# Optimization experiments

Hardware: AMD Instinct MI355X
Metric: run time of the kernel (lower is better)

Reference implementation:

```python
import jax, jax.numpy as jnp
import numpy as np

B, T, D, N = 64, 256, 32, 64  # batch, seq_len, input_dim, n_units
INIT_STD = 0.02


def setup_inputs() -> dict:
    key = jax.random.key(0)
    ks = jax.random.split(key, 13)
    x = jax.random.normal(ks[0], (B, T, D), dtype=jnp.float32)
    p = lambda k, shape: jax.random.normal(k, shape, dtype=jnp.float32) * INIT_STD
    return {
        "x": x,
        "W_j": p(ks[1], (D, N, N)), "W_i": p(ks[2], (D, N, N)),
        "W_f": p(ks[3], (D, N, N)), "W_o": p(ks[4], (D, N, N)),
        "U_j": p(ks[5], (D, 1, N)), "U_i": p(ks[6], (D, 1, N)),
        "U_f": p(ks[7], (D, 1, N)), "U_o": p(ks[8], (D, 1, N)),
        "b_j": p(ks[9], (D, N)), "b_i": p(ks[10], (D, N)),
        "b_f": p(ks[11], (D, N)), "b_o": p(ks[12], (D, N)),
    }


def reference(x, W_j, W_i, W_f, W_o, U_j, U_i, U_f, U_o, b_j, b_i, b_f, b_o):
    # x: [B, T, D]; per-input-variable LSTM with state [B, D, N].
    b = x.shape[0]
    d, _, n = W_j.shape
    # 'bij,jik->bjk' with i==1 is an outer product: x_t[b,d] * U[d,0,:]
    Uj, Ui, Uf, Uo = U_j[:, 0, :], U_i[:, 0, :], U_f[:, 0, :], U_o[:, 0, :]

    def step(carry, x_t):  # x_t: [B, D]
        h, c = carry  # each [B, D, N]
        xe = x_t[:, :, None]  # [B, D, 1]
        gate = lambda W, U, bb: jnp.einsum('bdn,dnm->bdm', h, W) + xe * U + bb
        j = jnp.tanh(gate(W_j, Uj, b_j))
        i = jax.nn.sigmoid(gate(W_i, Ui, b_i))
        f = jax.nn.sigmoid(gate(W_f, Uf, b_f))
        o = jax.nn.sigmoid(gate(W_o, Uo, b_o))
        c = c * f + i * j
        h = o * jnp.tanh(c)
        return (h, c), h

    h0 = jnp.zeros((b, d, n), dtype=x.dtype)
    (h_T, c_T), outs = jax.lax.scan(step, (h0, h0), jnp.swapaxes(x, 0, 1))
    outputs = jnp.swapaxes(outs, 0, 1)  # [B, T, D, N]
    return (outputs, (h_T, c_T))
```

## Files before the change

kernel.cpp:

```cpp
#include <hip/hip_runtime.h>
#include <hip/hip_bf16.h>
#include <stdint.h>


typedef __attribute__((ext_vector_type(8))) __bf16 bf16x8;
typedef __attribute__((ext_vector_type(4))) float f32x4;

union FragU { uint4 u; bf16x8 v; };

__device__ __forceinline__ float fast_sigmoid(float x) {
    float e = __builtin_amdgcn_exp2f(-1.4426950408889634f * x);
    return __builtin_amdgcn_rcpf(1.0f + e);
}
__device__ __forceinline__ float fast_tanh(float x) {
    float e = __builtin_amdgcn_exp2f(2.8853900817779268f * x);
    return 1.0f - 2.0f * __builtin_amdgcn_rcpf(1.0f + e);
}

__global__ __launch_bounds__(256, 2) void lstm_kernel(
    const float* __restrict__ x,
    const float* __restrict__ Wj, const float* __restrict__ Wi,
    const float* __restrict__ Wf, const float* __restrict__ Wo,
    const float* __restrict__ Uj, const float* __restrict__ Ui,
    const float* __restrict__ Uf, const float* __restrict__ Uo,
    const float* __restrict__ bj, const float* __restrict__ bi,
    const float* __restrict__ bf, const float* __restrict__ bo,
    float* __restrict__ out)
{
    constexpr int T = 256, D = 32, N = 64, B = 64;
    const int bid   = blockIdx.x;
    const int d     = bid >> 4;
    const int btile = bid & 15;
    const int tid   = threadIdx.x;
    const int w     = tid >> 6;
    const int lane  = tid & 63;
    const int g     = lane >> 4;
    const int li    = lane & 15;
    const int mcol  = w * 16 + li;

    __shared__ __align__(16) __bf16 hbuf[2][4][64];
    __shared__ float xs[4][256];

    for (int idx = tid; idx < 2 * 4 * 64; idx += 256)
        (&hbuf[0][0][0])[idx] = (__bf16)0.0f;
    for (int idx = tid; idx < 4 * 256; idx += 256) {
        int bl = idx >> 8, t = idx & 255;
        xs[bl][t] = x[((size_t)(btile * 4 + bl) * T + t) * D + d];
    }

    const float* Wg[4] = { Wj, Wi, Wf, Wo };
    const float* Ug[4] = { Uj, Ui, Uf, Uo };
    const float* Bg[4] = { bj, bi, bf, bo };
    FragU wfrag[4][2];
    float uv[4], bv[4];
    #pragma unroll
    for (int G = 0; G < 4; ++G) {
        uv[G] = Ug[G][d * N + mcol];
        bv[G] = Bg[G][d * N + mcol];
        const float* base = Wg[G] + (size_t)d * N * N + mcol;
        #pragma unroll
        for (int f = 0; f < 2; ++f) {
            const int k0 = f * 32 + g * 8;
            bf16x8 tmp;
            #pragma unroll
            for (int j = 0; j < 8; ++j)
                tmp[j] = (__bf16)base[(size_t)(k0 + j) * N];
            wfrag[G][f].v = tmp;
        }
    }

    f32x4 acc[4];
    #pragma unroll
    for (int G = 0; G < 4; ++G)
        acc[G] = f32x4{ bv[G], bv[G], bv[G], bv[G] };

    const int cm = mcol >> 3;
    const int woff = (((cm + 2 * g) & 7) << 3) | (mcol & 7);
    __bf16* hw0 = &hbuf[0][g][0] + woff;
    __bf16* hw1 = &hbuf[1][g][0] + woff;

    const int rr = li >> 2;
    const int p0 = (g + 2 * rr) & 7;
    const int p1 = (g + 4 + 2 * rr) & 7;
    const uint4* ra00 = (const uint4*)&hbuf[0][rr][p0 << 3];
    const uint4* ra01 = (const uint4*)&hbuf[1][rr][p0 << 3];
    const uint4* ra10 = (const uint4*)&hbuf[0][rr][p1 << 3];
    const uint4* ra11 = (const uint4*)&hbuf[1][rr][p1 << 3];

    __syncthreads();

    if (((bid >> 3) ^ (bid >> 8)) & 1)
        asm volatile("s_sleep 6" ::: "memory");

    float c0 = 0.f, h0 = 0.f;
    const int gb = btile * 4 + g;
    uint32_t oidx = (uint32_t)gb * (T * D * N) + (uint32_t)(d * N + mcol);

    #pragma unroll 1
    for (int t = 0; t < T; t += 8) {
        const float4 xa = *(const float4*)&xs[g][t];
        const float4 xb = *(const float4*)&xs[g][t + 4];
        #pragma unroll
        for (int uu = 0; uu < 8; ++uu) {
            __builtin_amdgcn_s_setprio(1);
            const int rb = uu & 1;
            FragU a0, a1;
            a0.u = *(rb ? ra01 : ra00);
            a1.u = *(rb ? ra11 : ra10);
            const float xv = (uu < 4) ? xa[uu] : xb[uu - 4];
            #pragma unroll
            for (int G = 0; G < 4; ++G)
                acc[G][0] = __builtin_fmaf(xv, uv[G], bv[G]);
            #pragma unroll
            for (int G = 0; G < 4; ++G) {
                acc[G] = __builtin_amdgcn_mfma_f32_16x16x32_bf16(a0.v, wfrag[G][0].v, acc[G], 0, 0, 0);
                acc[G] = __builtin_amdgcn_mfma_f32_16x16x32_bf16(a1.v, wfrag[G][1].v, acc[G], 0, 0, 0);
            }
            const float jj = fast_tanh   (acc[0][0]);
            const float ii = fast_sigmoid(acc[1][0]);
            const float ff = fast_sigmoid(acc[2][0]);
            const float oo = fast_sigmoid(acc[3][0]);
            c0 = __builtin_fmaf(c0, ff, ii * jj);
            h0 = oo * fast_tanh(c0);
            __builtin_amdgcn_s_setprio(0);
            *(rb ? hw0 : hw1) = (__bf16)h0;
            out[oidx] = h0;
            oidx += D * N;
            asm volatile("s_waitcnt lgkmcnt(0)" ::: "memory");
            __builtin_amdgcn_s_barrier();
        }
    }

    const size_t baseH = (size_t)B * T * D * N;
    const size_t baseC = baseH + (size_t)B * D * N;
    const size_t i0 = ((size_t)gb * D + d) * N + mcol;
    out[baseH + i0] = h0;
    out[baseC + i0] = c0;
}

extern "C" void kernel_launch(void* const* d_in, const int* in_sizes, int n_in,
                              void* d_out, int out_size, void* d_ws, size_t ws_size,
                              hipStream_t stream) {
    lstm_kernel<<<dim3(512), dim3(256), 0, stream>>>(
        (const float*)d_in[0],
        (const float*)d_in[1], (const float*)d_in[2],
        (const float*)d_in[3], (const float*)d_in[4],
        (const float*)d_in[5], (const float*)d_in[6],
        (const float*)d_in[7], (const float*)d_in[8],
        (const float*)d_in[9], (const float*)d_in[10],
        (const float*)d_in[11], (const float*)d_in[12],
        (float*)d_out);
}
```

Before: 80.46 us.

## Process eight batch rows per block using two MFMA accumulator rows

Each block now handles 8 batch rows instead of 4, so each thread carries two independent LSTM states in accumulator rows 0 and 1 of the same MFMA. The grid is halved to 256 blocks (one per CU on MI355X), the h buffer is padded to 72 columns in place of the XOR swizzle, and the setprio and staggered-sleep tricks are removed. This halves the number of serial recurrences per CU and doubles the useful rows per MFMA. In exchange each step does twice the gate math and global stores per thread, and occupancy is lower.

```diff
diff --git a/kernel.cpp b/kernel.cpp
--- a/kernel.cpp
+++ b/kernel.cpp
@@ -17,7 +17,7 @@
     return 1.0f - 2.0f * __builtin_amdgcn_rcpf(1.0f + e);
 }
 
-__global__ __launch_bounds__(256, 2) void lstm_kernel(
+__global__ __launch_bounds__(256, 1) void lstm_kernel(
     const float* __restrict__ x,
     const float* __restrict__ Wj, const float* __restrict__ Wi,
     const float* __restrict__ Wf, const float* __restrict__ Wo,
@@ -29,23 +29,23 @@
 {
     constexpr int T = 256, D = 32, N = 64, B = 64;
     const int bid   = blockIdx.x;
-    const int d     = bid >> 4;
-    const int btile = bid & 15;
+    const int d     = bid >> 3;
+    const int btile = bid & 7;
     const int tid   = threadIdx.x;
     const int w     = tid >> 6;
     const int lane  = tid & 63;
-    const int g     = lane >> 4;
+    const int q     = lane >> 4;
     const int li    = lane & 15;
     const int mcol  = w * 16 + li;
 
-    __shared__ __align__(16) __bf16 hbuf[2][4][64];
-    __shared__ float xs[4][256];
+    __shared__ __align__(16) __bf16 hbuf[2][8][72];
+    __shared__ __align__(16) float xs[8][256];
 
-    for (int idx = tid; idx < 2 * 4 * 64; idx += 256)
+    for (int idx = tid; idx < 2 * 8 * 72; idx += 256)
         (&hbuf[0][0][0])[idx] = (__bf16)0.0f;
-    for (int idx = tid; idx < 4 * 256; idx += 256) {
+    for (int idx = tid; idx < 8 * 256; idx += 256) {
         int bl = idx >> 8, t = idx & 255;
-        xs[bl][t] = x[((size_t)(btile * 4 + bl) * T + t) * D + d];
+        xs[bl][t] = x[((size_t)(btile * 8 + bl) * T + t) * D + d];
     }
 
     const float* Wg[4] = { Wj, Wi, Wf, Wo };
@@ -60,7 +60,7 @@
         const float* base = Wg[G] + (size_t)d * N * N + mcol;
         #pragma unroll
         for (int f = 0; f < 2; ++f) {
-            const int k0 = f * 32 + g * 8;
+            const int k0 = f * 32 + q * 8;
             bf16x8 tmp;
             #pragma unroll
             for (int j = 0; j < 8; ++j)
@@ -74,58 +74,68 @@
     for (int G = 0; G < 4; ++G)
         acc[G] = f32x4{ bv[G], bv[G], bv[G], bv[G] };
 
-    const int cm = mcol >> 3;
-    const int woff = (((cm + 2 * g) & 7) << 3) | (mcol & 7);
-    __bf16* hw0 = &hbuf[0][g][0] + woff;
-    __bf16* hw1 = &hbuf[1][g][0] + woff;
+    const int bb0 = 2 * q, bb1 = 2 * q + 1;
+    __bf16* hw0a = &hbuf[0][bb0][mcol];
+    __bf16* hw0b = &hbuf[0][bb1][mcol];
+    __bf16* hw1a = &hbuf[1][bb0][mcol];
+    __bf16* hw1b = &hbuf[1][bb1][mcol];
 
-    const int rr = li >> 2;
-    const int p0 = (g + 2 * rr) & 7;
-    const int p1 = (g + 4 + 2 * rr) & 7;
-    const uint4* ra00 = (const uint4*)&hbuf[0][rr][p0 << 3];
-    const uint4* ra01 = (const uint4*)&hbuf[1][rr][p0 << 3];
-    const uint4* ra10 = (const uint4*)&hbuf[0][rr][p1 << 3];
-    const uint4* ra11 = (const uint4*)&hbuf[1][rr][p1 << 3];
+    const int rr = 2 * (li >> 2) + (li & 1);
+    const uint4* ra00 = (const uint4*)&hbuf[0][rr][q * 8];
+    const uint4* ra01 = (const uint4*)&hbuf[1][rr][q * 8];
+    const uint4* ra10 = (const uint4*)&hbuf[0][rr][32 + q * 8];
+    const uint4* ra11 = (const uint4*)&hbuf[1][rr][32 + q * 8];
 
     __syncthreads();
 
-    if (((bid >> 3) ^ (bid >> 8)) & 1)
-        asm volatile("s_sleep 6" ::: "memory");
-
-    float c0 = 0.f, h0 = 0.f;
-    const int gb = btile * 4 + g;
-    uint32_t oidx = (uint32_t)gb * (T * D * N) + (uint32_t)(d * N + mcol);
+    float c0a = 0.f, h0a = 0.f, c0b = 0.f, h0b = 0.f;
+    const int gb0 = btile * 8 + bb0;
+    const int gb1 = gb0 + 1;
+    uint32_t oidx0 = (uint32_t)gb0 * (T * D * N) + (uint32_t)(d * N + mcol);
+    uint32_t oidx1 = (uint32_t)gb1 * (T * D * N) + (uint32_t)(d * N + mcol);
 
     #pragma unroll 1
     for (int t = 0; t < T; t += 8) {
-        const float4 xa = *(const float4*)&xs[g][t];
-        const float4 xb = *(const float4*)&xs[g][t + 4];
+        const float4 xa0 = *(const float4*)&xs[bb0][t];
+        const float4 xb0 = *(const float4*)&xs[bb0][t + 4];
+        const float4 xa1 = *(const float4*)&xs[bb1][t];
+        const float4 xb1 = *(const float4*)&xs[bb1][t + 4];
         #pragma unroll
         for (int uu = 0; uu < 8; ++uu) {
-            __builtin_amdgcn_s_setprio(1);
             const int rb = uu & 1;
             FragU a0, a1;
             a0.u = *(rb ? ra01 : ra00);
             a1.u = *(rb ? ra11 : ra10);
-            const float xv = (uu < 4) ? xa[uu] : xb[uu - 4];
+            const float xv0 = (uu < 4) ? xa0[uu] : xb0[uu - 4];
+            const float xv1 = (uu < 4) ? xa1[uu] : xb1[uu - 4];
             #pragma unroll
-            for (int G = 0; G < 4; ++G)
-                acc[G][0] = __builtin_fmaf(xv, uv[G], bv[G]);
+            for (int G = 0; G < 4; ++G) {
+                acc[G][0] = __builtin_fmaf(xv0, uv[G], bv[G]);
+                acc[G][1] = __builtin_fmaf(xv1, uv[G], bv[G]);
+            }
             #pragma unroll
             for (int G = 0; G < 4; ++G) {
                 acc[G] = __builtin_amdgcn_mfma_f32_16x16x32_bf16(a0.v, wfrag[G][0].v, acc[G], 0, 0, 0);
                 acc[G] = __builtin_amdgcn_mfma_f32_16x16x32_bf16(a1.v, wfrag[G][1].v, acc[G], 0, 0, 0);
             }
-            const float jj = fast_tanh   (acc[0][0]);
-            const float ii = fast_sigmoid(acc[1][0]);
-            const float ff = fast_sigmoid(acc[2][0]);
-            const float oo = fast_sigmoid(acc[3][0]);
-            c0 = __builtin_fmaf(c0, ff, ii * jj);
-            h0 = oo * fast_tanh(c0);
-            __builtin_amdgcn_s_setprio(0);
-            *(rb ? hw0 : hw1) = (__bf16)h0;
-            out[oidx] = h0;
-            oidx += D * N;
+            const float jja = fast_tanh   (acc[0][0]);
+            const float iia = fast_sigmoid(acc[1][0]);
+            const float ffa = fast_sigmoid(acc[2][0]);
+            const float ooa = fast_sigmoid(acc[3][0]);
+            c0a = __builtin_fmaf(c0a, ffa, iia * jja);
+            h0a = ooa * fast_tanh(c0a);
+            const float jjb = fast_tanh   (acc[0][1]);
+            const float iib = fast_sigmoid(acc[1][1]);
+            const float ffb = fast_sigmoid(acc[2][1]);
+            const float oob = fast_sigmoid(acc[3][1]);
+            c0b = __builtin_fmaf(c0b, ffb, iib * jjb);
+            h0b = oob * fast_tanh(c0b);
+            if (rb) { *hw0a = (__bf16)h0a; *hw0b = (__bf16)h0b; }
+            else    { *hw1a = (__bf16)h0a; *hw1b = (__bf16)h0b; }
+            out[oidx0] = h0a;
+            out[oidx1] = h0b;
+            oidx0 += D * N;
+            oidx1 += D * N;
             asm volatile("s_waitcnt lgkmcnt(0)" ::: "memory");
             __builtin_amdgcn_s_barrier();
         }
@@ -133,15 +143,18 @@
 
     const size_t baseH = (size_t)B * T * D * N;
     const size_t baseC = baseH + (size_t)B * D * N;
-    const size_t i0 = ((size_t)gb * D + d) * N + mcol;
-    out[baseH + i0] = h0;
-    out[baseC + i0] = c0;
+    const size_t i0 = ((size_t)gb0 * D + d) * N + mcol;
+    const size_t i1 = ((size_t)gb1 * D + d) * N + mcol;
+    out[baseH + i0] = h0a;
+    out[baseC + i0] = c0a;
+    out[baseH + i1] = h0b;
+    out[baseC + i1] = c0b;
 }
 
 extern "C" void kernel_launch(void* const* d_in, const int* in_sizes, int n_in,
                               void* d_out, int out_size, void* d_ws, size_t ws_size,
                               hipStream_t stream) {
-    lstm_kernel<<<dim3(512), dim3(256), 0, stream>>>(
+    lstm_kernel<<<dim3(256), dim3(256), 0, stream>>>(
         (const float*)d_in[0],
         (const float*)d_in[1], (const float*)d_in[2],
         (const float*)d_in[3], (const float*)d_in[4],
```

After: 98.19 us. 22.0% more time.
